# Kernel tuning notes

Hardware: AMD Instinct MI355X
Metric: run time of the kernel (lower is better)

Reference implementation:

```python
import jax, jax.numpy as jnp
import numpy as np

# hyperparams matching init_kwargs
T_LEN = 1024
T_LATENCY = 7
TB = T_LATENCY + 1          # t_len_block
N_OUT = 1024
BATCH = 32
FS_SCALE = 10.0             # FastSigmoid default scale


@jax.custom_vjp
def fast_sigmoid(x):
    # forward: Heaviside; backward: fast-sigmoid surrogate
    return (x > 0).astype(x.dtype)

def _fs_fwd(x):
    return (x > 0).astype(x.dtype), x

def _fs_bwd(x, g):
    return (g / (FS_SCALE * jnp.abs(x) + 1.0) ** 2,)

fast_sigmoid.defvjp(_fs_fwd, _fs_bwd)


def setup_inputs() -> dict:
    key = jax.random.key(0)
    k1, k2, k3, k4 = jax.random.split(key, 4)
    x = jax.random.normal(k1, (T_LEN, BATCH, N_OUT), dtype=jnp.float32) * 0.6
    # raw params; forward applies the clamp/abs 'properties' of the module
    beta_raw = jax.random.uniform(k2, (N_OUT,), minval=0.7, maxval=0.99, dtype=jnp.float32)
    p_raw = jax.random.uniform(k3, (N_OUT,), minval=0.5, maxval=0.95, dtype=jnp.float32)
    b_raw = jax.random.uniform(k4, (N_OUT,), minval=0.2, maxval=1.0, dtype=jnp.float32)
    return {"x": x, "beta_raw": beta_raw, "p_raw": p_raw, "b_raw": b_raw}


def reference(x, beta_raw, p_raw, b_raw):
    T, B, N = x.shape
    tb = TB
    n_blocks = T // tb  # t_pad == 0 by construction
    dt = x.dtype

    # clamped properties
    beta = jnp.clip(beta_raw, 0.001, 0.999)          # [N]
    p = jnp.clip(jnp.abs(p_raw), 0.0, 0.999)         # [N]
    bb = jnp.clip(jnp.abs(b_raw), 0.001, 1.0)        # [N]

    t_idx = jnp.arange(tb)
    expo = t_idx[:, None] - t_idx[None, :]            # [tb,tb], t - s
    lower = expo >= 0
    # causal decay kernel: beta^(t-s) for s<=t  (grouped conv1d equivalent)
    beta_pow = jnp.where(lower[:, :, None],
                         beta[None, None, :] ** jnp.maximum(expo, 0)[:, :, None].astype(dt),
                         jnp.zeros((), dt))           # [tb,tb,N]
    # phi kernel: weight (t-s+1) for s<=t  (conv2d equivalent)
    phi = jnp.where(lower, (expo + 1).astype(dt), jnp.zeros((), dt))  # [tb,tb]
    p_exp = jnp.arange(1, tb + 1, dtype=dt)           # [tb]
    p_pow = p[None, :] ** p_exp[:, None]              # [tb,N]
    inv_p = 1.0 / p                                   # [N]

    def body(carry, x_slice):
        spikes, z, int_mem, a_kernel = carry          # [tb,B,N],[tb,B,N],[B,N],[tb,B,N]
        sg = jax.lax.stop_gradient(spikes)            # detach_spike_grad=True
        maskf = (jnp.max(sg, axis=0) > 0).astype(dt)  # [B,N] any spike in prev block
        # refractory masking of input
        xs = jnp.where(z < maskf[None], jnp.zeros((), dt), x_slice)
        v_init = int_mem * (1.0 - maskf)
        # adaptation update
        a_at_spike = jnp.sum(a_kernel * sg, axis=0) + inv_p          # [B,N]
        decay_steps = jnp.sum(z > 1, axis=0).astype(dt)              # [B,N]
        new_a = a_at_spike * jnp.power(p[None, :], decay_steps)
        a = a_kernel[-1] * (1.0 - maskf) + new_a * maskf             # [B,N]
        a_k = p_pow[:, None, :] * a[None]                             # [tb,B,N]
        v_th = 1.0 + bb[None, None, :] * a_k                          # [tb,B,N]
        # --- Block forward ---
        cur = xs.at[0].add(beta[None, :] * v_init)
        membrane = jnp.einsum('tsn,sbn->tbn', beta_pow, cur)          # causal decayed sum
        faulty = fast_sigmoid(membrane - v_th)                        # [tb,B,N] 0/1
        z_new = jnp.einsum('ts,sbn->tbn', phi, faulty)
        # g(): keep only entries exactly 1, straight-through grad
        spikes_new = z_new - jax.lax.stop_gradient(
            jnp.where(z_new == 1.0, jnp.zeros((), dt), z_new))
        return (spikes_new, z_new, membrane[-1], a_k), spikes_new

    z0 = jnp.zeros((tb, B, N), dt)
    carry0 = (z0, z0, jnp.zeros((B, N), dt), z0)
    xb = x.reshape(n_blocks, tb, B, N)
    _, out = jax.lax.scan(body, carry0, xb)
    return out.reshape(T, B, N)
```

## Files before the change

### kernel.cpp

```cpp
#include <hip/hip_runtime.h>


constexpr int T_LEN = 1024;
constexpr int TB    = 8;
constexpr int NBLK  = T_LEN / TB;
constexpr int BATCH = 32;
constexpr int NOUT  = 1024;
constexpr int BN    = BATCH * NOUT;
constexpr int PF    = 4;
constexpr int SLOTS = 5;

#define WAITVM(N) asm volatile("s_waitcnt vmcnt(" #N ")" ::: "memory")

typedef const __attribute__((address_space(1))) void* gptr_t;
typedef __attribute__((address_space(3))) void*       sptr_t;

__global__ __launch_bounds__(64, 1)
void snn_blocks_kernel(const float* __restrict__ x,
                       const float* __restrict__ beta_raw,
                       const float* __restrict__ p_raw,
                       const float* __restrict__ b_raw,
                       float* __restrict__ out)
{
    __shared__ float lds[SLOTS][TB][64];

    const int lane = threadIdx.x;
    const int gid  = blockIdx.x * 64 + lane;
    const int n    = gid & (NOUT - 1);

    double beta = (double)beta_raw[n];
    beta = beta < 0.001 ? 0.001 : (beta > 0.999 ? 0.999 : beta);
    double p = fabs((double)p_raw[n]);
    p = p > 0.999 ? 0.999 : p;
    double bb = fabs((double)b_raw[n]);
    bb = bb < 0.001 ? 0.001 : (bb > 1.0 ? 1.0 : bb);
    const double inv_p = 1.0 / p;

    double ppow[9];
    ppow[0] = 1.0;
#pragma unroll
    for (int i = 1; i <= 8; ++i) ppow[i] = ppow[i - 1] * p;

    double bbp[8];
#pragma unroll
    for (int t = 0; t < 8; ++t) bbp[t] = bb * ppow[t + 1];

    double m = 0.0;
    double a = 0.0;
    int    maskf = 0;
    int    decay = 0;
    double ssum  = 0.0;
    int    zzero = 0xFF;

    const float* xg = x + gid;
    float*       og = out + gid;

#pragma unroll
    for (int k = 0; k < PF; ++k) {
#pragma unroll
        for (int t = 0; t < TB; ++t) {
            __builtin_amdgcn_global_load_lds(
                (gptr_t)(xg + (ptrdiff_t)(k * TB + t) * BN),
                (sptr_t)&lds[k][t][0], 4, 0, 0);
        }
    }

    int rs = 0;
    int ws = PF % SLOTS;

    auto body = [&](int blk) {
        float cur[8];
#pragma unroll
        for (int t = 0; t < 8; ++t) cur[t] = lds[rs][t][lane];

        const double a_at = a * ssum + inv_p;
        double pd = 1.0;
        pd *= (decay & 1) ? p       : 1.0;
        pd *= (decay & 2) ? ppow[2] : 1.0;
        pd *= (decay & 4) ? ppow[4] : 1.0;
        pd *= (decay & 8) ? ppow[8] : 1.0;
        const double new_a = a_at * pd;

        if (maskf) { a = new_a;     m = 0.0; }
        else       { a = ppow[8] * a;        }

        int nmaskf = 0, ndecay = 0, nzzero = 0;
        double nssum = 0.0;
        int c = 0, zc = 0;
        float* o = og + (ptrdiff_t)blk * TB * BN;
#pragma unroll
        for (int t = 0; t < 8; ++t) {
            double xv = (double)cur[t];
            if (maskf && ((zzero >> t) & 1)) xv = 0.0;
            m = beta * m + xv;
            const double vth = 1.0 + bbp[t] * a;
            const int f = (m - vth > 0.0) ? 1 : 0;
            c  += f;
            zc += c;
            nmaskf |= (zc == 1);
            ndecay += (zc > 1) ? 1 : 0;
            nssum  += (zc == 1) ? ppow[t + 1] : 0.0;
            nzzero |= (zc == 0) ? (1 << t) : 0;
            __builtin_nontemporal_store((zc == 1) ? 1.0f : 0.0f,
                                        o + (ptrdiff_t)t * BN);
        }
        maskf = nmaskf; decay = ndecay; ssum = nssum; zzero = nzzero;

        const int pfb = blk + PF;
        if (pfb < NBLK) {
#pragma unroll
            for (int t = 0; t < TB; ++t) {
                __builtin_amdgcn_global_load_lds(
                    (gptr_t)(xg + (ptrdiff_t)(pfb * TB + t) * BN),
                    (sptr_t)&lds[ws][t][0], 4, 0, 0);
            }
        }
        if (++rs == SLOTS) rs = 0;
        if (++ws == SLOTS) ws = 0;
    };

    WAITVM(24); body(0);
    WAITVM(32); body(1);
    WAITVM(40); body(2);
    for (int blk = 3; blk < NBLK - PF; ++blk) {
        WAITVM(48);
        body(blk);
    }
    for (int blk = NBLK - PF; blk < NBLK; ++blk) {
        WAITVM(16);
        body(blk);
    }
}

extern "C" void kernel_launch(void* const* d_in, const int* in_sizes, int n_in,
                              void* d_out, int out_size, void* d_ws, size_t ws_size,
                              hipStream_t stream) {
    const float* x        = (const float*)d_in[0];
    const float* beta_raw = (const float*)d_in[1];
    const float* p_raw    = (const float*)d_in[2];
    const float* b_raw    = (const float*)d_in[3];
    float* out            = (float*)d_out;

    dim3 grid(BN / 64);
    dim3 block(64);
    snn_blocks_kernel<<<grid, block, 0, stream>>>(x, beta_raw, p_raw, b_raw, out);
}
```

Before: 246.5 us.

## Use 16-byte global-to-LDS loads, LDS-staged vector stores, and deeper prefetch

Input loads now use 16-byte global_load_lds: each lane fetches four consecutive floats across rows and time steps, so there are 2 load instructions per block instead of 8. Outputs go into a small LDS buffer and are then written as two float4 nontemporal stores per lane rather than eight scalar stores. The prefetch depth rises from 4 to 8 blocks, and the vmcnt waits are retuned to match. This cuts memory instruction count and raises bytes in flight per wave, at the cost of an extra LDS round trip and lgkmcnt wait on the output path, plus a more delicate vmcnt accounting.

```diff
diff --git a/kernel.cpp b/kernel.cpp
--- a/kernel.cpp
+++ b/kernel.cpp
@@ -7,13 +7,15 @@
 constexpr int BATCH = 32;
 constexpr int NOUT  = 1024;
 constexpr int BN    = BATCH * NOUT;
-constexpr int PF    = 4;
-constexpr int SLOTS = 5;
+constexpr int PF    = 8;
+constexpr int SLOTS = 9;
 
-#define WAITVM(N) asm volatile("s_waitcnt vmcnt(" #N ")" ::: "memory")
+#define WAITVM(N)  asm volatile("s_waitcnt vmcnt(" #N ")" ::: "memory")
+#define WAITLGKM0  asm volatile("s_waitcnt lgkmcnt(0)" ::: "memory")
 
 typedef const __attribute__((address_space(1))) void* gptr_t;
 typedef __attribute__((address_space(3))) void*       sptr_t;
+typedef float f4 __attribute__((ext_vector_type(4)));
 
 __global__ __launch_bounds__(64, 1)
 void snn_blocks_kernel(const float* __restrict__ x,
@@ -22,11 +24,16 @@
                        const float* __restrict__ b_raw,
                        float* __restrict__ out)
 {
-    __shared__ float lds[SLOTS][TB][64];
+    __shared__ float ldsin[SLOTS][TB][64];
+    __shared__ float sbuf[TB][64];
 
     const int lane = threadIdx.x;
-    const int gid  = blockIdx.x * 64 + lane;
+    const int wg0  = blockIdx.x * 64;
+    const int gid  = wg0 + lane;
     const int n    = gid & (NOUT - 1);
+
+    const int rowoff = lane >> 4;
+    const int coloff = wg0 + (lane & 15) * 4;
 
     double beta = (double)beta_raw[n];
     beta = beta < 0.001 ? 0.001 : (beta > 0.999 ? 0.999 : beta);
@@ -52,16 +59,14 @@
     double ssum  = 0.0;
     int    zzero = 0xFF;
 
-    const float* xg = x + gid;
-    float*       og = out + gid;
-
 #pragma unroll
     for (int k = 0; k < PF; ++k) {
 #pragma unroll
-        for (int t = 0; t < TB; ++t) {
-            __builtin_amdgcn_global_load_lds(
-                (gptr_t)(xg + (ptrdiff_t)(k * TB + t) * BN),
-                (sptr_t)&lds[k][t][0], 4, 0, 0);
+        for (int h = 0; h < 2; ++h) {
+            const float* src = x + (ptrdiff_t)(k * TB + h * 4 + rowoff) * BN + coloff;
+            __builtin_amdgcn_global_load_lds((gptr_t)src,
+                                             (sptr_t)&ldsin[k][h * 4][0],
+                                             16, 0, 0);
         }
     }
 
@@ -71,7 +76,7 @@
     auto body = [&](int blk) {
         float cur[8];
 #pragma unroll
-        for (int t = 0; t < 8; ++t) cur[t] = lds[rs][t][lane];
+        for (int t = 0; t < 8; ++t) cur[t] = ldsin[rs][t][lane];
 
         const double a_at = a * ssum + inv_p;
         double pd = 1.0;
@@ -87,7 +92,6 @@
         int nmaskf = 0, ndecay = 0, nzzero = 0;
         double nssum = 0.0;
         int c = 0, zc = 0;
-        float* o = og + (ptrdiff_t)blk * TB * BN;
 #pragma unroll
         for (int t = 0; t < 8; ++t) {
             double xv = (double)cur[t];
@@ -101,33 +105,49 @@
             ndecay += (zc > 1) ? 1 : 0;
             nssum  += (zc == 1) ? ppow[t + 1] : 0.0;
             nzzero |= (zc == 0) ? (1 << t) : 0;
-            __builtin_nontemporal_store((zc == 1) ? 1.0f : 0.0f,
-                                        o + (ptrdiff_t)t * BN);
+            sbuf[t][lane] = (zc == 1) ? 1.0f : 0.0f;
         }
         maskf = nmaskf; decay = ndecay; ssum = nssum; zzero = nzzero;
+
+        WAITLGKM0;
+        {
+            const float* sflat = &sbuf[0][0];
+            f4 v0 = *(const f4*)(sflat + lane * 4);
+            f4 v1 = *(const f4*)(sflat + 256 + lane * 4);
+            float* d0 = out + (ptrdiff_t)(blk * TB + rowoff) * BN + coloff;
+            float* d1 = out + (ptrdiff_t)(blk * TB + 4 + rowoff) * BN + coloff;
+            __builtin_nontemporal_store(v0, (f4*)d0);
+            __builtin_nontemporal_store(v1, (f4*)d1);
+        }
 
         const int pfb = blk + PF;
         if (pfb < NBLK) {
 #pragma unroll
-            for (int t = 0; t < TB; ++t) {
-                __builtin_amdgcn_global_load_lds(
-                    (gptr_t)(xg + (ptrdiff_t)(pfb * TB + t) * BN),
-                    (sptr_t)&lds[ws][t][0], 4, 0, 0);
+            for (int h = 0; h < 2; ++h) {
+                const float* src = x + (ptrdiff_t)(pfb * TB + h * 4 + rowoff) * BN + coloff;
+                __builtin_amdgcn_global_load_lds((gptr_t)src,
+                                                 (sptr_t)&ldsin[ws][h * 4][0],
+                                                 16, 0, 0);
             }
         }
         if (++rs == SLOTS) rs = 0;
         if (++ws == SLOTS) ws = 0;
     };
 
-    WAITVM(24); body(0);
-    WAITVM(32); body(1);
-    WAITVM(40); body(2);
-    for (int blk = 3; blk < NBLK - PF; ++blk) {
-        WAITVM(48);
+    WAITVM(14); body(0);
+    WAITVM(16); body(1);
+    WAITVM(18); body(2);
+    WAITVM(20); body(3);
+    WAITVM(22); body(4);
+    WAITVM(24); body(5);
+    WAITVM(26); body(6);
+    WAITVM(28); body(7);
+    for (int blk = PF; blk < NBLK - PF; ++blk) {
+        WAITVM(28);
         body(blk);
     }
     for (int blk = NBLK - PF; blk < NBLK; ++blk) {
-        WAITVM(16);
+        WAITVM(14);
         body(blk);
     }
 }
```

Measured after the change: 298.1 us. +20.9%, slower.

## Use a deep register prefetch ring with dwordx4 loads and stores staged via LDS

Applied to the files above, without the earlier changes.

Replaces the per-timestep scalar global_load_lds prefetch with 128-bit global loads into a 16-deep register ring. Each block's data is transposed through LDS so every lane still processes one neuron. Outputs are also staged in LDS and written back as 128-bit nontemporal stores instead of eight scalar stores. The aim is to cut the number of memory instructions and keep more bytes in flight per wave, at the cost of more VGPRs, extra LDS traffic, and hand-counted vmcnt waits that must also account for the stores.

```diff
diff --git a/kernel.cpp b/kernel.cpp
--- a/kernel.cpp
+++ b/kernel.cpp
@@ -7,13 +7,16 @@
 constexpr int BATCH = 32;
 constexpr int NOUT  = 1024;
 constexpr int BN    = BATCH * NOUT;
-constexpr int PF    = 4;
-constexpr int SLOTS = 5;
+constexpr int PF    = 16;
 
-#define WAITVM(N) asm volatile("s_waitcnt vmcnt(" #N ")" ::: "memory")
+typedef float f4 __attribute__((ext_vector_type(4)));
 
-typedef const __attribute__((address_space(1))) void* gptr_t;
-typedef __attribute__((address_space(3))) void*       sptr_t;
+#define WAITVM_T(N, A, B) \
+    asm volatile("s_waitcnt vmcnt(" #N ")" : "+v"(A), "+v"(B) :: "memory")
+
+#define GLOAD(DST, ADDR) \
+    asm volatile("global_load_dwordx4 %0, %1, off" \
+                 : "=v"(DST) : "v"(ADDR) : "memory")
 
 __global__ __launch_bounds__(64, 1)
 void snn_blocks_kernel(const float* __restrict__ x,
@@ -22,11 +25,16 @@
                        const float* __restrict__ b_raw,
                        float* __restrict__ out)
 {
-    __shared__ float lds[SLOTS][TB][64];
+    __shared__ float inbuf[TB][64];
+    __shared__ float sbuf[TB][64];
 
     const int lane = threadIdx.x;
-    const int gid  = blockIdx.x * 64 + lane;
+    const int wg0  = blockIdx.x * 64;
+    const int gid  = wg0 + lane;
     const int n    = gid & (NOUT - 1);
+
+    const int rowoff = lane >> 4;
+    const int coloff = wg0 + (lane & 15) * 4;
 
     double beta = (double)beta_raw[n];
     beta = beta < 0.001 ? 0.001 : (beta > 0.999 ? 0.999 : beta);
@@ -52,26 +60,20 @@
     double ssum  = 0.0;
     int    zzero = 0xFF;
 
-    const float* xg = x + gid;
-    float*       og = out + gid;
+    f4 fr[PF][2];
 
 #pragma unroll
     for (int k = 0; k < PF; ++k) {
-#pragma unroll
-        for (int t = 0; t < TB; ++t) {
-            __builtin_amdgcn_global_load_lds(
-                (gptr_t)(xg + (ptrdiff_t)(k * TB + t) * BN),
-                (sptr_t)&lds[k][t][0], 4, 0, 0);
-        }
+        GLOAD(fr[k][0], x + (ptrdiff_t)(k * TB + rowoff) * BN + coloff);
+        GLOAD(fr[k][1], x + (ptrdiff_t)(k * TB + 4 + rowoff) * BN + coloff);
     }
 
-    int rs = 0;
-    int ws = PF % SLOTS;
-
-    auto body = [&](int blk) {
+    auto body = [&](int blk, f4 v0, f4 v1) {
+        *(f4*)&inbuf[rowoff][(lane & 15) * 4]     = v0;
+        *(f4*)&inbuf[rowoff + 4][(lane & 15) * 4] = v1;
         float cur[8];
 #pragma unroll
-        for (int t = 0; t < 8; ++t) cur[t] = lds[rs][t][lane];
+        for (int t = 0; t < 8; ++t) cur[t] = inbuf[t][lane];
 
         const double a_at = a * ssum + inv_p;
         double pd = 1.0;
@@ -87,7 +89,6 @@
         int nmaskf = 0, ndecay = 0, nzzero = 0;
         double nssum = 0.0;
         int c = 0, zc = 0;
-        float* o = og + (ptrdiff_t)blk * TB * BN;
 #pragma unroll
         for (int t = 0; t < 8; ++t) {
             double xv = (double)cur[t];
@@ -101,35 +102,43 @@
             ndecay += (zc > 1) ? 1 : 0;
             nssum  += (zc == 1) ? ppow[t + 1] : 0.0;
             nzzero |= (zc == 0) ? (1 << t) : 0;
-            __builtin_nontemporal_store((zc == 1) ? 1.0f : 0.0f,
-                                        o + (ptrdiff_t)t * BN);
+            sbuf[t][lane] = (zc == 1) ? 1.0f : 0.0f;
         }
         maskf = nmaskf; decay = ndecay; ssum = nssum; zzero = nzzero;
 
-        const int pfb = blk + PF;
-        if (pfb < NBLK) {
-#pragma unroll
-            for (int t = 0; t < TB; ++t) {
-                __builtin_amdgcn_global_load_lds(
-                    (gptr_t)(xg + (ptrdiff_t)(pfb * TB + t) * BN),
-                    (sptr_t)&lds[ws][t][0], 4, 0, 0);
-            }
-        }
-        if (++rs == SLOTS) rs = 0;
-        if (++ws == SLOTS) ws = 0;
+        const float* sflat = &sbuf[0][0];
+        f4 s0 = *(const f4*)(sflat + lane * 4);
+        f4 s1 = *(const f4*)(sflat + 256 + lane * 4);
+        __builtin_nontemporal_store(
+            s0, (f4*)(out + (ptrdiff_t)(blk * TB + rowoff) * BN + coloff));
+        __builtin_nontemporal_store(
+            s1, (f4*)(out + (ptrdiff_t)(blk * TB + 4 + rowoff) * BN + coloff));
     };
 
-    WAITVM(24); body(0);
-    WAITVM(32); body(1);
-    WAITVM(40); body(2);
-    for (int blk = 3; blk < NBLK - PF; ++blk) {
-        WAITVM(48);
-        body(blk);
+#define STEP(N, BLK, SL) do {                                              \
+        WAITVM_T(N, fr[SL][0], fr[SL][1]);                                 \
+        body((BLK), fr[SL][0], fr[SL][1]);                                 \
+        const int pfb = (BLK) + PF;                                        \
+        GLOAD(fr[SL][0], x + (ptrdiff_t)(pfb * TB + rowoff) * BN + coloff);\
+        GLOAD(fr[SL][1], x + (ptrdiff_t)(pfb * TB + 4 + rowoff) * BN + coloff);\
+    } while (0)
+
+#define STEPT(N, BLK, SL) do {                                             \
+        WAITVM_T(N, fr[SL][0], fr[SL][1]);                                 \
+        body((BLK), fr[SL][0], fr[SL][1]);                                 \
+    } while (0)
+
+#pragma unroll
+    for (int j = 0; j < 16; ++j) STEP(30, j, j);
+
+#pragma unroll 1
+    for (int r = 1; r < 7; ++r) {
+#pragma unroll
+        for (int i = 0; i < 16; ++i) STEP(60, r * 16 + i, i);
     }
-    for (int blk = NBLK - PF; blk < NBLK; ++blk) {
-        WAITVM(16);
-        body(blk);
-    }
+
+#pragma unroll
+    for (int k = 0; k < 16; ++k) STEPT(30, 112 + k, k);
 }
 
 extern "C" void kernel_launch(void* const* d_in, const int* in_sizes, int n_in,
```

New measurement: 250.9 us. Within noise of the previous version (+1.8%).
